# Kernel optimization log

Hardware: AMD Instinct MI355X
Metric: run time of the kernel (lower is better)

Reference implementation:

```python
import jax, jax.numpy as jnp
import numpy as np
from jax import lax

INV_SQRT2 = np.float32(1.0 / np.sqrt(2.0))

def conv2d(x, w, b=None, stride=1, pad=0):
    y = lax.conv_general_dilated(x, w, (stride, stride), [(pad, pad), (pad, pad)],
                                 dimension_numbers=('NCHW', 'OIHW', 'NCHW'))
    return y if b is None else y + b[None, :, None, None]

def haar_dwt2_zero(x):
    # pytorch_wavelets DWTForward(J=1, wave='haar', mode='zero') for odd H,W:
    # pad one zero at the end of each spatial dim, then pairwise Haar analysis.
    x = jnp.pad(x, ((0, 0), (0, 0), (0, 1), (0, 1)))
    xe, xo = x[..., 0::2], x[..., 1::2]
    lo_w, hi_w = (xe + xo) * INV_SQRT2, (xe - xo) * INV_SQRT2
    def rows(t):
        te, to = t[:, :, 0::2, :], t[:, :, 1::2, :]
        return (te + to) * INV_SQRT2, (te - to) * INV_SQRT2
    ll, lh = rows(lo_w)
    hl, hh = rows(hi_w)
    return ll, lh, hl, hh  # cA, cH, cV, cD

def pixel_shuffle2(x):
    B, C, H, W = x.shape
    co = C // 4
    return x.reshape(B, co, 2, 2, H, W).transpose(0, 1, 4, 2, 5, 3).reshape(B, co, H * 2, W * 2)

def gaussian_kernel5(sigma=0.5):
    r = np.arange(5, dtype=np.float64) - 2.0
    k = np.exp(-(r ** 2) / (2.0 * sigma * sigma))
    return jnp.asarray((k / k.sum()).astype(np.float32))

_GK = gaussian_kernel5(0.5)

def gaussian_blur5(x4d):
    # cv2.GaussianBlur ksize=(5,5) sigma=0.5, default BORDER_REFLECT_101 -> 'reflect' pad
    p = jnp.pad(x4d, ((0, 0), (0, 0), (2, 2), (2, 2)), mode='reflect')
    p = conv2d(p, _GK.reshape(1, 1, 5, 1))
    return conv2d(p, _GK.reshape(1, 1, 1, 5))

def channel_attention(x, w1, w2):
    avg = jnp.mean(x, axis=(2, 3), keepdims=True)
    mx = jnp.max(x, axis=(2, 3), keepdims=True)
    mlp = lambda v: conv2d(jax.nn.relu(conv2d(v, w1)), w2)
    return jax.nn.sigmoid(mlp(avg) + mlp(mx)) * x

def _forward(x, w_x1, b_x1, w_x2, b_x2, w_x3, b_x3, w_hi, b_hi, w_lo, b_lo,
             ca1_w1, ca1_w2, ca2_w1, ca2_w2, w_cat, b_cat, w_c9a, b_c9a, w_c9b, b_c9b):
    f1 = jax.nn.relu(conv2d(x, w_x1, b_x1))            # (1,16,H,W)
    f2 = jax.nn.relu(conv2d(f1, w_x2, b_x2))           # (1,8,H,W)
    tmp12 = jax.nn.relu(conv2d(f2, w_x3, b_x3))        # (1,1,H,W)
    cA, cH, cV, cD = haar_dwt2_zero(tmp12)             # each (1,1,(H+1)/2,(W+1)/2)
    hf = pixel_shuffle2(jax.nn.relu(conv2d(jnp.concatenate([cH, cV, cD], 1), w_hi, b_hi, pad=1)))
    lf = pixel_shuffle2(jax.nn.relu(conv2d(cA, w_lo, b_lo, pad=1)))  # (1,1,H+5,W+5)
    # original detaches hf (cpu->numpy->cv2->cuda): gradients do not flow through it
    hf = gaussian_blur5(lax.stop_gradient(hf))
    hf = channel_attention(hf, ca1_w1, ca1_w2)
    lf = channel_attention(lf, ca2_w1, ca2_w2)
    alpha = 1.0
    cat = jax.nn.relu(conv2d(jnp.concatenate([alpha * hf, (1.0 - alpha) * lf], 1), w_cat, b_cat))
    f12 = tmp12 + cat                                   # (1,1,H,W)
    h = jax.nn.relu(conv2d(f12, w_c9a, b_c9a, pad=1))   # (1,32,H,W)
    return jax.nn.relu(conv2d(h, w_c9b, b_c9b, pad=1))  # (1,64,H,W)

def setup_inputs() -> dict:
    key = jax.random.key(0)
    ks = jax.random.split(key, 24)
    f32 = jnp.float32
    n = lambda k, s, sc=0.05: jax.random.normal(k, s, f32) * sc
    H = W = 511
    return {
        'x': jax.random.normal(ks[0], (1, 204, H, W), f32),
        'w_x1': n(ks[1], (16, 204, 1, 1)), 'b_x1': n(ks[2], (16,)),
        'w_x2': n(ks[3], (8, 16, 1, 1)),   'b_x2': n(ks[4], (8,)),
        'w_x3': n(ks[5], (1, 8, 1, 1)),    'b_x3': n(ks[6], (1,)),
        'w_hi': n(ks[7], (4, 3, 1, 1)),    'b_hi': n(ks[8], (4,)),
        'w_lo': n(ks[9], (4, 1, 1, 1)),    'b_lo': n(ks[10], (4,)),
        'ca1_w1': n(ks[11], (1, 1, 1, 1), 0.5), 'ca1_w2': n(ks[12], (1, 1, 1, 1), 0.5),
        'ca2_w1': n(ks[13], (1, 1, 1, 1), 0.5), 'ca2_w2': n(ks[14], (1, 1, 1, 1), 0.5),
        'w_cat': n(ks[15], (1, 2, 6, 6)),  'b_cat': n(ks[16], (1,)),
        'w_c9a': n(ks[17], (32, 1, 3, 3)), 'b_c9a': n(ks[18], (32,)),
        'w_c9b': n(ks[19], (64, 32, 3, 3)), 'b_c9b': n(ks[20], (64,)),
    }

def reference(x, w_x1, b_x1, w_x2, b_x2, w_x3, b_x3, w_hi, b_hi, w_lo, b_lo,
              ca1_w1, ca1_w2, ca2_w1, ca2_w2, w_cat, b_cat, w_c9a, b_c9a, w_c9b, b_c9b):
    return _forward(x, w_x1, b_x1, w_x2, b_x2, w_x3, b_x3, w_hi, b_hi, w_lo, b_lo,
                    ca1_w1, ca1_w2, ca2_w1, ca2_w2, w_cat, b_cat, w_c9a, b_c9a, w_c9b, b_c9b)
```

## Files before the change

### kernel.cpp

```cpp
#include <hip/hip_runtime.h>
#include <hip/hip_bf16.h>
#include <math.h>

#define NP    261121
#define WPX   520
#define ROWN  4160
#define PSTR  2138240
#define NBLUR 1041

typedef __attribute__((ext_vector_type(8))) short short8;
typedef __attribute__((ext_vector_type(4))) float f32x4;
typedef __attribute__((ext_vector_type(4), aligned(4))) float f32x4a;

static __device__ __forceinline__ unsigned short f2bf(float f) {
    unsigned int u = __builtin_bit_cast(unsigned int, f);
    u += 0x7FFFu + ((u >> 16) & 1u);
    return (unsigned short)(u >> 16);
}

static __device__ __forceinline__ short bf16s(float f) {
    __hip_bfloat16 h = __float2bfloat16(f);
    return __builtin_bit_cast(short, h);
}

__global__ __launch_bounds__(256, 3) void k_conv123(const float* __restrict__ x,
                                                    const float* __restrict__ w_x1,
                                                    const float* __restrict__ b1,
                                                    const float* __restrict__ w2,
                                                    const float* __restrict__ b2,
                                                    const float* __restrict__ w3,
                                                    const float* __restrict__ b3,
                                                    float* __restrict__ tmp12)
{
    int lane = threadIdx.x & 63, wave = threadIdx.x >> 6;
    int lpx = lane & 15, kg = lane >> 4;
    int s = blockIdx.x * 4 + wave;
    int pxb = s * 64;
    if (pxb > NP - 64) pxb = NP - 64;

    short8 afr[7];
    {
        const float* wrow = w_x1 + lpx * 204;
#pragma unroll
        for (int ks = 0; ks < 7; ++ks)
#pragma unroll
            for (int j = 0; j < 8; ++j) {
                int c = ks * 32 + kg * 8 + j;
                float wv = (c < 204) ? wrow[c] : 0.f;
                afr[ks][j] = (short)f2bf(wv);
            }
    }

    const float* pj[8];
#pragma unroll
    for (int j = 0; j < 8; ++j)
        pj[j] = x + (size_t)(kg * 8 + j) * NP + pxb + lpx * 4;

    f32x4 acc[4];
#pragma unroll
    for (int n = 0; n < 4; ++n) acc[n] = (f32x4){0.f, 0.f, 0.f, 0.f};

    f32x4a qA[8], qB[8];

#define LOADKS(Q, KS) do { \
        _Pragma("unroll") \
        for (int j = 0; j < 8; ++j) { \
            const size_t o = ((KS) < 6 || kg * 8 + j < 12) ? (size_t)(KS) * 32 * NP : 0; \
            Q[j] = *reinterpret_cast<const f32x4a*>(pj[j] + o); \
        } \
    } while (0)

#define PROC(Q, KS) do { \
        short8 bfr[4]; \
        _Pragma("unroll") \
        for (int n = 0; n < 4; ++n) \
            _Pragma("unroll") \
            for (int j = 0; j < 8; ++j) \
                bfr[n][j] = bf16s(Q[j][n]); \
        _Pragma("unroll") \
        for (int n = 0; n < 4; ++n) \
            acc[n] = __builtin_amdgcn_mfma_f32_16x16x32_bf16(afr[KS], bfr[n], acc[n], 0, 0, 0); \
    } while (0)

    LOADKS(qA, 0);
    LOADKS(qB, 1);
    PROC(qA, 0);
    LOADKS(qA, 2);
    PROC(qB, 1);
    LOADKS(qB, 3);
    PROC(qA, 2);
    LOADKS(qA, 4);
    PROC(qB, 3);
    LOADKS(qB, 5);
    PROC(qA, 4);
    LOADKS(qA, 6);
    PROC(qB, 5);
    PROC(qA, 6);
#undef LOADKS
#undef PROC

    float4 b1v = *reinterpret_cast<const float4*>(b1 + kg * 4);
    float4 w2v[8];
#pragma unroll
    for (int j = 0; j < 8; ++j)
        w2v[j] = *reinterpret_cast<const float4*>(w2 + j * 16 + kg * 4);
    float b2v[8], w3v[8];
#pragma unroll
    for (int j = 0; j < 8; ++j) { b2v[j] = b2[j]; w3v[j] = w3[j]; }
    float b3v = b3[0];

    f32x4 resv;
#pragma unroll
    for (int n = 0; n < 4; ++n) {
        float f0 = fmaxf(acc[n][0] + b1v.x, 0.f);
        float f1 = fmaxf(acc[n][1] + b1v.y, 0.f);
        float f2 = fmaxf(acc[n][2] + b1v.z, 0.f);
        float f3 = fmaxf(acc[n][3] + b1v.w, 0.f);
        float tmp = b3v;
#pragma unroll
        for (int j = 0; j < 8; ++j) {
            float sj = f0 * w2v[j].x;
            sj = fmaf(f1, w2v[j].y, sj);
            sj = fmaf(f2, w2v[j].z, sj);
            sj = fmaf(f3, w2v[j].w, sj);
            sj += __shfl_xor(sj, 16, 64);
            sj += __shfl_xor(sj, 32, 64);
            tmp = fmaf(fmaxf(sj + b2v[j], 0.f), w3v[j], tmp);
        }
        resv[n] = fmaxf(tmp, 0.f);
    }
    if (kg == 0)
        *reinterpret_cast<f32x4a*>(tmp12 + pxb + lpx * 4) = resv;
}

__global__ __launch_bounds__(256) void k_dwt(const float* __restrict__ tmp12,
                                             const float* __restrict__ w_hi,
                                             const float* __restrict__ b_hi,
                                             const float* __restrict__ w_c9b,
                                             float* __restrict__ hf,
                                             unsigned short* __restrict__ wb2,
                                             unsigned short* __restrict__ h2)
{
    int t = blockIdx.x * 256 + threadIdx.x;

    if (t < 18432) {
        int o = t / 288, ck = t - o * 288;
        int c = ck / 9, k = ck - c * 9;
        wb2[k * 2048 + o * 32 + c] = f2bf(w_c9b[t]);
    }
    short8 z8 = {0, 0, 0, 0, 0, 0, 0, 0};
    if (t < 4160) {
        int pl = t / 1040;
        int rr = t - pl * 1040;
        int row = rr >= 520 ? 512 : 0;
        int ch  = rr >= 520 ? rr - 520 : rr;
        *reinterpret_cast<short8*>(h2 + (size_t)pl * PSTR + (size_t)row * ROWN + ch * 8) = z8;
    }
    int z = t - 4160;
    if (z >= 0 && z < 6132) {
        int row = z / 12 + 1;
        int j = z - (row - 1) * 12;
        int pl = j / 3, cidx = j - pl * 3;
        int col = (cidx == 0) ? 0 : (cidx == 1 ? 512 : 513);
        *reinterpret_cast<short8*>(h2 + (size_t)pl * PSTR + (size_t)row * ROWN + col * 8) = z8;
    }

    const float INV = 0.70710678118654752440f;
    if (t >= 258 * 258) return;
    int h = t / 258, w = t - h * 258;

    float wh[12], bh[4];
#pragma unroll
    for (int i = 0; i < 12; ++i) wh[i] = w_hi[i];
#pragma unroll
    for (int o = 0; o < 4; ++o) bh[o] = b_hi[o];

    float v[4];
    if (h == 0 || h == 257 || w == 0 || w == 257) {
#pragma unroll
        for (int o = 0; o < 4; ++o) v[o] = fmaxf(bh[o], 0.f);
    } else {
        int hh = h - 1, ww = w - 1;
        int r0 = 2 * hh, r1 = 2 * hh + 1, c0 = 2 * ww, c1 = 2 * ww + 1;
        float a = tmp12[r0 * 511 + c0];
        float b = (c1 < 511) ? tmp12[r0 * 511 + c1] : 0.f;
        float c = (r1 < 511) ? tmp12[r1 * 511 + c0] : 0.f;
        float d = (r1 < 511 && c1 < 511) ? tmp12[r1 * 511 + c1] : 0.f;
        float lo0 = (a + b) * INV, hi0 = (a - b) * INV;
        float lo1 = (c + d) * INV, hi1 = (c - d) * INV;
        float cH = (lo0 - lo1) * INV;
        float cV = (hi0 + hi1) * INV;
        float cD = (hi0 - hi1) * INV;
#pragma unroll
        for (int o = 0; o < 4; ++o)
            v[o] = fmaxf(wh[o * 3 + 0] * cH + wh[o * 3 + 1] * cV + wh[o * 3 + 2] * cD + bh[o], 0.f);
    }
    int orow = (2 * h) * 516 + 2 * w;
    hf[orow]       = v[0];
    hf[orow + 1]   = v[1];
    hf[orow + 516] = v[2];
    hf[orow + 517] = v[3];
}

__global__ __launch_bounds__(256) void k_blur(const float* __restrict__ hf,
                                              float* __restrict__ hfb,
                                              float* __restrict__ psum,
                                              float* __restrict__ pmax,
                                              float g0, float g1, float g2)
{
    __shared__ float ss[256], sm[256];
    int t = threadIdx.x;
    int idx = blockIdx.x * 256 + t;
    bool ok = idx < 516 * 516;
    int idc = ok ? idx : 0;
    int y = idc / 516, x = idc - y * 516;
    float g[5] = {g0, g1, g2, g1, g0};
    int ry[5], rx[5];
#pragma unroll
    for (int i = 0; i < 5; ++i) {
        int yy = y + i - 2; yy = yy < 0 ? -yy : (yy > 515 ? 1030 - yy : yy);
        int xx = x + i - 2; xx = xx < 0 ? -xx : (xx > 515 ? 1030 - xx : xx);
        ry[i] = yy * 516; rx[i] = xx;
    }
    float s = 0.f;
#pragma unroll
    for (int i = 0; i < 5; ++i) {
        float rs = 0.f;
#pragma unroll
        for (int j = 0; j < 5; ++j) rs = fmaf(g[j], hf[ry[i] + rx[j]], rs);
        s = fmaf(g[i], rs, s);
    }
    if (ok) hfb[idx] = s;

    ss[t] = ok ? s : 0.f;
    sm[t] = ok ? s : -3.4e38f;
    __syncthreads();
    for (int off = 128; off > 0; off >>= 1) {
        if (t < off) { ss[t] += ss[t + off]; sm[t] = fmaxf(sm[t], sm[t + off]); }
        __syncthreads();
    }
    if (t == 0) { psum[blockIdx.x] = ss[0]; pmax[blockIdx.x] = sm[0]; }
}

__global__ __launch_bounds__(256) void k_cat(const float* __restrict__ hfb,
                                             const float* __restrict__ tmp12,
                                             const float* __restrict__ psum,
                                             const float* __restrict__ pmax,
                                             const float* __restrict__ caw1,
                                             const float* __restrict__ caw2,
                                             const float* __restrict__ w_cat,
                                             const float* __restrict__ b_cat,
                                             float* __restrict__ f12)
{
    __shared__ float ss[256], sm[256], ssc;
    int t = threadIdx.x;
    {
        float s = 0.f, m = -3.4e38f;
        for (int i = t; i < NBLUR; i += 256) { s += psum[i]; m = fmaxf(m, pmax[i]); }
        ss[t] = s; sm[t] = m;
        __syncthreads();
        for (int off = 128; off > 0; off >>= 1) {
            if (t < off) { ss[t] += ss[t + off]; sm[t] = fmaxf(sm[t], sm[t + off]); }
            __syncthreads();
        }
        if (t == 0) {
            float avg = ss[0] / 266256.f;
            float a = caw1[0], b = caw2[0];
            float z = b * fmaxf(a * avg, 0.f) + b * fmaxf(a * sm[0], 0.f);
            ssc = 1.f / (1.f + expf(-z));
        }
        __syncthreads();
    }
    float sc = ssc;

    int p = blockIdx.x * 256 + t;
    if (p >= NP) return;
    int y = p / 511, x = p - y * 511;
    float s = 0.f;
#pragma unroll
    for (int ky = 0; ky < 6; ++ky) {
        const float* row = hfb + (y + ky) * 516 + x;
#pragma unroll
        for (int kx = 0; kx < 6; ++kx) s = fmaf(row[kx], w_cat[ky * 6 + kx], s);
    }
    f12[p] = tmp12[p] + fmaxf(sc * s + b_cat[0], 0.f);
}

__global__ __launch_bounds__(256) void k_c9a(const float* __restrict__ f12,
                                             const float* __restrict__ w_c9a,
                                             const float* __restrict__ bias,
                                             unsigned short* __restrict__ h2)
{
    int p = blockIdx.x * 256 + threadIdx.x;
    if (p >= NP) return;
    int y = p / 511, x = p - y * 511;
    float hv[9];
#pragma unroll
    for (int ky = 0; ky < 3; ++ky)
#pragma unroll
        for (int kx = 0; kx < 3; ++kx) {
            int yy = y + ky - 1, xx = x + kx - 1;
            hv[ky * 3 + kx] = (yy >= 0 && yy < 511 && xx >= 0 && xx < 511) ? f12[yy * 511 + xx] : 0.f;
        }
    float acc[32];
#pragma unroll
    for (int o = 0; o < 32; ++o) acc[o] = bias[o];
#pragma unroll
    for (int k = 0; k < 9; ++k) {
        float v = hv[k];
#pragma unroll
        for (int o = 0; o < 32; ++o) acc[o] = fmaf(v, w_c9a[o * 9 + k], acc[o]);
    }
    unsigned short o16[32];
#pragma unroll
    for (int o = 0; o < 32; ++o) o16[o] = f2bf(fmaxf(acc[o], 0.f));
    size_t px = (size_t)(y + 1) * WPX + (x + 1);
#pragma unroll
    for (int i = 0; i < 4; ++i)
        *reinterpret_cast<short8*>(h2 + (size_t)i * PSTR + px * 8) =
            reinterpret_cast<const short8*>(o16)[i];
}

__global__ __launch_bounds__(256, 3) void k_c9b(const unsigned short* __restrict__ h2,
                                                const unsigned short* __restrict__ wb2,
                                                const float* __restrict__ bias,
                                                float* __restrict__ out)
{
    __shared__ unsigned short swu[9 * 2048];

    int bid = blockIdx.x;
    int xcd = bid & 7, jj = bid >> 3;
    const int q = 127, r = 6;
    int wg = (xcd < r ? xcd * (q + 1) : r * (q + 1) + (xcd - r) * q) + jj;

    int lane = threadIdx.x & 63;
    int wave = threadIdx.x >> 6;
    int y  = wg >> 1;
    int xh = wg & 1;
    int xb = xh * 256 + wave * 64;
    int lpx = lane & 15, kg = lane >> 4;

    {
        const short8* wsrc = reinterpret_cast<const short8*>(wb2);
        short8* wdst = reinterpret_cast<short8*>(swu);
        for (int d = threadIdx.x; d < 2304; d += 256) {
            int kt = d >> 8, rem = d & 255, m = rem >> 6, l = rem & 63;
            wdst[d] = wsrc[kt * 256 + (m * 16 + (l & 15)) * 4 + (l >> 4)];
        }
    }
    __syncthreads();

    f32x4 acc[4][4];
#pragma unroll
    for (int m = 0; m < 4; ++m)
#pragma unroll
        for (int n = 0; n < 4; ++n) acc[m][n] = (f32x4){0.f, 0.f, 0.f, 0.f};

    const unsigned short* hb = h2 + (size_t)kg * PSTR;
    const int base_px = (y + 1) * WPX + (xb + 1) + lpx;
    const int rowm = base_px - WPX, row0 = base_px, rowp = base_px + WPX;
    const short8* swv = reinterpret_cast<const short8*>(swu);

#define LOADB(BUF, ROW, DX) do { \
        const unsigned short* rp = hb + (size_t)((ROW) + (DX)) * 8; \
        BUF[0] = *reinterpret_cast<const short8*>(rp); \
        BUF[1] = *reinterpret_cast<const short8*>(rp + 128); \
        BUF[2] = *reinterpret_cast<const short8*>(rp + 256); \
        BUF[3] = *reinterpret_cast<const short8*>(rp + 384); \
    } while (0)

#define TAP(KT, BUF) do { \
        const short8* ap = swv + (KT) * 256 + lane; \
        short8 a0 = ap[0], a1 = ap[64], a2 = ap[128], a3 = ap[192]; \
        _Pragma("unroll") \
        for (int n = 0; n < 4; ++n) { \
            acc[0][n] = __builtin_amdgcn_mfma_f32_16x16x32_bf16(a0, BUF[n], acc[0][n], 0, 0, 0); \
            acc[1][n] = __builtin_amdgcn_mfma_f32_16x16x32_bf16(a1, BUF[n], acc[1][n], 0, 0, 0); \
            acc[2][n] = __builtin_amdgcn_mfma_f32_16x16x32_bf16(a2, BUF[n], acc[2][n], 0, 0, 0); \
            acc[3][n] = __builtin_amdgcn_mfma_f32_16x16x32_bf16(a3, BUF[n], acc[3][n], 0, 0, 0); \
        } \
    } while (0)

    short8 bX[4], bY[4], bZ[4];
    LOADB(bX, rowm, -1);
    LOADB(bY, rowm,  0);
    LOADB(bZ, rowm, +1); TAP(0, bX);
    LOADB(bX, row0, -1); TAP(1, bY);
    LOADB(bY, row0,  0); TAP(2, bZ);
    LOADB(bZ, row0, +1); TAP(3, bX);
    LOADB(bX, rowp, -1); TAP(4, bY);
    LOADB(bY, rowp,  0); TAP(5, bZ);
    LOADB(bZ, rowp, +1); TAP(6, bX);
    TAP(7, bY);
    TAP(8, bZ);
#undef LOADB
#undef TAP

    const int ybase = y * 511;
#pragma unroll
    for (int m = 0; m < 4; ++m) {
#pragma unroll
        for (int rr = 0; rr < 4; ++rr) {
            int o = m * 16 + kg * 4 + rr;
            float bo = bias[o];
#pragma unroll
            for (int n = 0; n < 4; ++n) {
                int px = xb + n * 16 + lpx;
                if (px < 511)
                    out[(size_t)o * NP + ybase + px] = fmaxf(acc[m][n][rr] + bo, 0.f);
            }
        }
    }
}

extern "C" void kernel_launch(void* const* d_in, const int* in_sizes, int n_in,
                              void* d_out, int out_size, void* d_ws, size_t ws_size,
                              hipStream_t stream)
{
    (void)in_sizes; (void)n_in; (void)out_size; (void)ws_size;

    const float* x     = (const float*)d_in[0];
    const float* w_x1  = (const float*)d_in[1];
    const float* b_x1  = (const float*)d_in[2];
    const float* w_x2  = (const float*)d_in[3];
    const float* b_x2  = (const float*)d_in[4];
    const float* w_x3  = (const float*)d_in[5];
    const float* b_x3  = (const float*)d_in[6];
    const float* w_hi  = (const float*)d_in[7];
    const float* b_hi  = (const float*)d_in[8];
    const float* ca1w1 = (const float*)d_in[11];
    const float* ca1w2 = (const float*)d_in[12];
    const float* w_cat = (const float*)d_in[15];
    const float* b_cat = (const float*)d_in[16];
    const float* w_c9a = (const float*)d_in[17];
    const float* b_c9a = (const float*)d_in[18];
    const float* w_c9b = (const float*)d_in[19];
    const float* b_c9b = (const float*)d_in[20];

    float* ws    = (float*)d_ws;
    float* tmp12 = ws + 0;
    float* hf    = ws + 261184;
    float* hfb   = ws + 527488;
    float* f12   = ws + 793792;
    float* psum  = ws + 1054976;
    float* pmax  = ws + 1056032;
    unsigned short* wb2 = (unsigned short*)(ws + 1057088);
    unsigned short* h2  = (unsigned short*)(ws + 1066304);

    float* out = (float*)d_out;

    double kk[5], ssum = 0.0;
    for (int i = 0; i < 5; ++i) { double r = i - 2.0; kk[i] = exp(-r * r / 0.5); ssum += kk[i]; }
    float g0 = (float)(kk[0] / ssum), g1 = (float)(kk[1] / ssum), g2 = (float)(kk[2] / ssum);

    k_conv123<<<1021, 256, 0, stream>>>(x, w_x1, b_x1, w_x2, b_x2, w_x3, b_x3, tmp12);
    k_dwt<<<261, 256, 0, stream>>>(tmp12, w_hi, b_hi, w_c9b, hf, wb2, h2);
    k_blur<<<NBLUR, 256, 0, stream>>>(hf, hfb, psum, pmax, g0, g1, g2);
    k_cat<<<1021, 256, 0, stream>>>(hfb, tmp12, psum, pmax, ca1w1, ca1w2, w_cat, b_cat, f12);
    k_c9a<<<1021, 256, 0, stream>>>(f12, w_c9a, b_c9a, h2);
    k_c9b<<<1022, 256, 0, stream>>>(h2, wb2, b_c9b, out);
}
```

Measured before the change: 115.9 us.

## Make conv123 persistent with atomic work-stealing over 64-pixel strips

```diff
diff --git a/kernel.cpp b/kernel.cpp
--- a/kernel.cpp
+++ b/kernel.cpp
@@ -3,6 +3,7 @@
 #include <math.h>
 
 #define NP    261121
+#define NST   4081
 #define WPX   520
 #define ROWN  4160
 #define PSTR  2138240
@@ -30,13 +31,11 @@
                                                     const float* __restrict__ b2,
                                                     const float* __restrict__ w3,
                                                     const float* __restrict__ b3,
-                                                    float* __restrict__ tmp12)
-{
-    int lane = threadIdx.x & 63, wave = threadIdx.x >> 6;
+                                                    float* __restrict__ tmp12,
+                                                    unsigned int* __restrict__ counter)
+{
+    int lane = threadIdx.x & 63;
     int lpx = lane & 15, kg = lane >> 4;
-    int s = blockIdx.x * 4 + wave;
-    int pxb = s * 64;
-    if (pxb > NP - 64) pxb = NP - 64;
 
     short8 afr[7];
     {
@@ -46,27 +45,34 @@
 #pragma unroll
             for (int j = 0; j < 8; ++j) {
                 int c = ks * 32 + kg * 8 + j;
-                float wv = (c < 204) ? wrow[c] : 0.f;
-                afr[ks][j] = (short)f2bf(wv);
+                afr[ks][j] = (short)f2bf(c < 204 ? wrow[c] : 0.f);
             }
     }
 
-    const float* pj[8];
+    const float* bj[8];
 #pragma unroll
     for (int j = 0; j < 8; ++j)
-        pj[j] = x + (size_t)(kg * 8 + j) * NP + pxb + lpx * 4;
-
-    f32x4 acc[4];
-#pragma unroll
-    for (int n = 0; n < 4; ++n) acc[n] = (f32x4){0.f, 0.f, 0.f, 0.f};
-
-    f32x4a qA[8], qB[8];
+        bj[j] = x + (size_t)(kg * 8 + j) * NP + lpx * 4;
+
+    while (true) {
+        int sv = 0;
+        if (lane == 0) sv = (int)atomicAdd(counter, 1u);
+        sv = __shfl(sv, 0, 64);
+        if (sv >= NST) break;
+        int pxb = sv * 64;
+        if (pxb > NP - 64) pxb = NP - 64;
+
+        f32x4 acc[4];
+#pragma unroll
+        for (int n = 0; n < 4; ++n) acc[n] = (f32x4){0.f, 0.f, 0.f, 0.f};
+
+        f32x4a qA[8], qB[8];
 
 #define LOADKS(Q, KS) do { \
         _Pragma("unroll") \
         for (int j = 0; j < 8; ++j) { \
             const size_t o = ((KS) < 6 || kg * 8 + j < 12) ? (size_t)(KS) * 32 * NP : 0; \
-            Q[j] = *reinterpret_cast<const f32x4a*>(pj[j] + o); \
+            Q[j] = *reinterpret_cast<const f32x4a*>(bj[j] + o + pxb); \
         } \
     } while (0)
 
@@ -82,55 +88,49 @@
             acc[n] = __builtin_amdgcn_mfma_f32_16x16x32_bf16(afr[KS], bfr[n], acc[n], 0, 0, 0); \
     } while (0)
 
-    LOADKS(qA, 0);
-    LOADKS(qB, 1);
-    PROC(qA, 0);
-    LOADKS(qA, 2);
-    PROC(qB, 1);
-    LOADKS(qB, 3);
-    PROC(qA, 2);
-    LOADKS(qA, 4);
-    PROC(qB, 3);
-    LOADKS(qB, 5);
-    PROC(qA, 4);
-    LOADKS(qA, 6);
-    PROC(qB, 5);
-    PROC(qA, 6);
+        LOADKS(qA, 0);
+        LOADKS(qB, 1);
+        PROC(qA, 0);
+        LOADKS(qA, 2);
+        PROC(qB, 1);
+        LOADKS(qB, 3);
+        PROC(qA, 2);
+        LOADKS(qA, 4);
+        PROC(qB, 3);
+        LOADKS(qB, 5);
+        PROC(qA, 4);
+        LOADKS(qA, 6);
+        PROC(qB, 5);
+        PROC(qA, 6);
 #undef LOADKS
 #undef PROC
 
-    float4 b1v = *reinterpret_cast<const float4*>(b1 + kg * 4);
-    float4 w2v[8];
-#pragma unroll
-    for (int j = 0; j < 8; ++j)
-        w2v[j] = *reinterpret_cast<const float4*>(w2 + j * 16 + kg * 4);
-    float b2v[8], w3v[8];
-#pragma unroll
-    for (int j = 0; j < 8; ++j) { b2v[j] = b2[j]; w3v[j] = w3[j]; }
-    float b3v = b3[0];
-
-    f32x4 resv;
-#pragma unroll
-    for (int n = 0; n < 4; ++n) {
-        float f0 = fmaxf(acc[n][0] + b1v.x, 0.f);
-        float f1 = fmaxf(acc[n][1] + b1v.y, 0.f);
-        float f2 = fmaxf(acc[n][2] + b1v.z, 0.f);
-        float f3 = fmaxf(acc[n][3] + b1v.w, 0.f);
-        float tmp = b3v;
-#pragma unroll
-        for (int j = 0; j < 8; ++j) {
-            float sj = f0 * w2v[j].x;
-            sj = fmaf(f1, w2v[j].y, sj);
-            sj = fmaf(f2, w2v[j].z, sj);
-            sj = fmaf(f3, w2v[j].w, sj);
-            sj += __shfl_xor(sj, 16, 64);
-            sj += __shfl_xor(sj, 32, 64);
-            tmp = fmaf(fmaxf(sj + b2v[j], 0.f), w3v[j], tmp);
-        }
-        resv[n] = fmaxf(tmp, 0.f);
-    }
-    if (kg == 0)
-        *reinterpret_cast<f32x4a*>(tmp12 + pxb + lpx * 4) = resv;
+        float4 b1v = *reinterpret_cast<const float4*>(b1 + kg * 4);
+        float b3v = b3[0];
+        f32x4 resv;
+#pragma unroll
+        for (int n = 0; n < 4; ++n) {
+            float f0 = fmaxf(acc[n][0] + b1v.x, 0.f);
+            float f1 = fmaxf(acc[n][1] + b1v.y, 0.f);
+            float f2 = fmaxf(acc[n][2] + b1v.z, 0.f);
+            float f3 = fmaxf(acc[n][3] + b1v.w, 0.f);
+            float tmp = b3v;
+#pragma unroll
+            for (int j = 0; j < 8; ++j) {
+                float4 w2v = *reinterpret_cast<const float4*>(w2 + j * 16 + kg * 4);
+                float sj = f0 * w2v.x;
+                sj = fmaf(f1, w2v.y, sj);
+                sj = fmaf(f2, w2v.z, sj);
+                sj = fmaf(f3, w2v.w, sj);
+                sj += __shfl_xor(sj, 16, 64);
+                sj += __shfl_xor(sj, 32, 64);
+                tmp = fmaf(fmaxf(sj + b2[j], 0.f), w3[j], tmp);
+            }
+            resv[n] = fmaxf(tmp, 0.f);
+        }
+        if (kg == 0)
+            *reinterpret_cast<f32x4a*>(tmp12 + pxb + lpx * 4) = resv;
+    }
 }
 
 __global__ __launch_bounds__(256) void k_dwt(const float* __restrict__ tmp12,
@@ -446,6 +446,7 @@
     float* pmax  = ws + 1056032;
     unsigned short* wb2 = (unsigned short*)(ws + 1057088);
     unsigned short* h2  = (unsigned short*)(ws + 1066304);
+    unsigned int* counter = (unsigned int*)(ws + 5342784);
 
     float* out = (float*)d_out;
 
@@ -453,7 +454,8 @@
     for (int i = 0; i < 5; ++i) { double r = i - 2.0; kk[i] = exp(-r * r / 0.5); ssum += kk[i]; }
     float g0 = (float)(kk[0] / ssum), g1 = (float)(kk[1] / ssum), g2 = (float)(kk[2] / ssum);
 
-    k_conv123<<<1021, 256, 0, stream>>>(x, w_x1, b_x1, w_x2, b_x2, w_x3, b_x3, tmp12);
+    hipMemsetAsync(counter, 0, 4, stream);
+    k_conv123<<<768, 256, 0, stream>>>(x, w_x1, b_x1, w_x2, b_x2, w_x3, b_x3, tmp12, counter);
     k_dwt<<<261, 256, 0, stream>>>(tmp12, w_hi, b_hi, w_c9b, hf, wb2, h2);
     k_blur<<<NBLUR, 256, 0, stream>>>(hf, hfb, psum, pmax, g0, g1, g2);
     k_cat<<<1021, 256, 0, stream>>>(hfb, tmp12, psum, pmax, ca1w1, ca1w2, w_cat, b_cat, f12);
```

Result: slower. 180.1 us (+55.4%).
